# Performance work log

Measured on AMD Instinct MI355X. Metric: run time of the kernel, lower is better.

Reference implementation:

```python
import jax, jax.numpy as jnp
import numpy as np

NODE_DIM = 128
HIDDEN = 64
N_NODES = 2048


def setup_inputs() -> dict:
    key = jax.random.key(0)
    ks = jax.random.split(key, 7)
    s_enc = 1.0 / np.sqrt(NODE_DIM)
    s1 = 1.0 / np.sqrt(2 * HIDDEN)
    s2 = 1.0 / np.sqrt(HIDDEN)
    return {
        "node_features": jax.random.normal(ks[0], (N_NODES, NODE_DIM), dtype=jnp.float32),
        "W_enc": jax.random.uniform(ks[1], (NODE_DIM, HIDDEN), jnp.float32, -s_enc, s_enc),
        "b_enc": jax.random.uniform(ks[2], (HIDDEN,), jnp.float32, -s_enc, s_enc),
        "W1": jax.random.uniform(ks[3], (2 * HIDDEN, HIDDEN), jnp.float32, -s1, s1),
        "b1": jax.random.uniform(ks[4], (HIDDEN,), jnp.float32, -s1, s1),
        "W2": jax.random.uniform(ks[5], (HIDDEN, 1), jnp.float32, -s2, s2),
        "b2": jax.random.uniform(ks[6], (1,), jnp.float32, -s2, s2),
    }


def reference(node_features, W_enc, b_enc, W1, b1, W2, b2):
    # node encoder: (n, node_dim) -> (n, hidden)
    h = node_features @ W_enc + b_enc
    # split first edge-MLP weight into the halves acting on h_i and h_j of the concat
    Wa, Wb = W1[:HIDDEN], W1[HIDDEN:]
    a = h @ Wa  # (n, hidden) contribution from source node i
    b = h @ Wb  # (n, hidden) contribution from target node j
    # pairwise pre-activation: (n, n, hidden) == Linear(concat(h_i, h_j))
    z = jax.nn.relu(a[:, None, :] + b[None, :, :] + b1)
    logits = jnp.einsum("ijh,ho->ijo", z, W2)[..., 0] + b2[0]  # (n, n)
    T = jax.nn.sigmoid(logits)
    # diagonal is never written in the original loop -> stays 0
    n = T.shape[0]
    return T * (1.0 - jnp.eye(n, dtype=T.dtype))
```

## Files before the change

kernel.cpp:

```cpp
#include <hip/hip_runtime.h>
#include <math.h>

#define NODE_DIM 128
#define HIDDEN   64
#define NN       2048

typedef float v4f __attribute__((ext_vector_type(4)));

__global__ __launch_bounds__(256) void prep_kernel(
    const float* __restrict__ nf, const float* __restrict__ W_enc,
    const float* __restrict__ b_enc, const float* __restrict__ W1,
    const float* __restrict__ b1, float* __restrict__ A, float* __restrict__ BB)
{
    __shared__ float nf_s[4][NODE_DIM];
    __shared__ float h_s[4][HIDDEN];
    const int tid = threadIdx.x;
    const int rg  = tid >> 6;
    const int t   = tid & 63;
    const int r   = blockIdx.x * 4 + rg;

    ((float2*)nf_s[rg])[t] = ((const float2*)(nf + (size_t)r * NODE_DIM))[t];
    __syncthreads();

    float acc = b_enc[t];
    #pragma unroll 8
    for (int k = 0; k < NODE_DIM; ++k)
        acc = fmaf(nf_s[rg][k], W_enc[k * HIDDEN + t], acc);
    h_s[rg][t] = acc;
    __syncthreads();

    float aacc = 0.0f;
    float bacc = b1[t];
    #pragma unroll 8
    for (int k = 0; k < HIDDEN; ++k) {
        const float hv = h_s[rg][k];
        aacc = fmaf(hv, W1[k * HIDDEN + t], aacc);
        bacc = fmaf(hv, W1[(HIDDEN + k) * HIDDEN + t], bacc);
    }
    A[(size_t)r * HIDDEN + t]  = aacc;
    BB[(size_t)r * HIDDEN + t] = bacc;
}

__global__ __launch_bounds__(256) void pair_kernel(
    const float* __restrict__ A, const float* __restrict__ BB,
    const float* __restrict__ W2, const float* __restrict__ b2,
    float* __restrict__ out)
{
    __shared__ float aL[64][68];
    __shared__ float bT[64][68];
    __shared__ float w2s[HIDDEN];

    const int tid = threadIdx.x;
    const int i0  = blockIdx.y * 64;
    const int j0  = blockIdx.x * 64;

    const float4* ga = (const float4*)(A  + (size_t)i0 * HIDDEN);
    const float4* gb = (const float4*)(BB + (size_t)j0 * HIDDEN);
    #pragma unroll
    for (int k = 0; k < 4; ++k) {
        const int idx = tid + k * 256;
        const int e   = idx * 4;
        const int row = e >> 6;
        const int col = e & 63;
        const float4 va = ga[idx];
        const float4 vb = gb[idx];
        *(float4*)&aL[row][col] = va;
        bT[col + 0][row] = vb.x;
        bT[col + 1][row] = vb.y;
        bT[col + 2][row] = vb.z;
        bT[col + 3][row] = vb.w;
    }
    if (tid < HIDDEN) w2s[tid] = W2[tid];
    __syncthreads();

    const int ty = tid >> 4;
    const int tx = tid & 15;

    float acc[4][4] = {{0.0f}};

    #pragma unroll 4
    for (int h = 0; h < HIDDEN; h += 4) {
        const v4f w = *(const v4f*)&w2s[h];
        v4f av[4], bv[4];
        #pragma unroll
        for (int ii = 0; ii < 4; ++ii)
            av[ii] = *(const v4f*)&aL[ty * 4 + ii][h];
        #pragma unroll
        for (int hh = 0; hh < 4; ++hh)
            bv[hh] = *(const v4f*)&bT[h + hh][tx * 4];
        #pragma unroll
        for (int ii = 0; ii < 4; ++ii) {
            #pragma unroll
            for (int jj = 0; jj < 4; ++jj) {
                float s = acc[ii][jj];
                #pragma unroll
                for (int hh = 0; hh < 4; ++hh)
                    s = fmaf(fmaxf(av[ii][hh] + bv[hh][jj], 0.0f), w[hh], s);
                acc[ii][jj] = s;
            }
        }
    }

    const float bias2 = b2[0];
    #pragma unroll
    for (int ii = 0; ii < 4; ++ii) {
        const int i = i0 + ty * 4 + ii;
        v4f o;
        #pragma unroll
        for (int jj = 0; jj < 4; ++jj) {
            const int j = j0 + tx * 4 + jj;
            const float x  = acc[ii][jj] + bias2;
            const float sg = 1.0f / (1.0f + __expf(-x));
            o[jj] = (i == j) ? 0.0f : sg;
        }
        *(v4f*)&out[(size_t)i * NN + (j0 + tx * 4)] = o;
    }
}

extern "C" void kernel_launch(void* const* d_in, const int* in_sizes, int n_in,
                              void* d_out, int out_size, void* d_ws, size_t ws_size,
                              hipStream_t stream) {
    const float* nf    = (const float*)d_in[0];
    const float* W_enc = (const float*)d_in[1];
    const float* b_enc = (const float*)d_in[2];
    const float* W1    = (const float*)d_in[3];
    const float* b1    = (const float*)d_in[4];
    const float* W2    = (const float*)d_in[5];
    const float* b2    = (const float*)d_in[6];
    float* out = (float*)d_out;

    float* A  = (float*)d_ws;
    float* BB = A + (size_t)NN * HIDDEN;

    prep_kernel<<<NN / 4, 256, 0, stream>>>(nf, W_enc, b_enc, W1, b1, A, BB);
    pair_kernel<<<dim3(32, 32), 256, 0, stream>>>(A, BB, W2, b2, out);
}
```

Before: 101.3 us.

## Use 128x128 pair tiles with 8x8 per-thread outputs and packed float2 math

The pair kernel moves from 64x64 to 128x128 output tiles, and each thread now computes an 8x8 strided block. The hidden-dimension inner loop uses two-wide vector add, max and multiply, which aims at the packed FP32 instructions, and it keeps two partial sums per output. B is now stored row-major instead of transposed, W2 is read directly from global memory, and launch bounds ask for 2 waves per SIMD. The goal is more arithmetic per shared-memory load and higher ALU throughput, at the cost of many more registers and strided scalar output stores that replace the vectorized stores.

```diff
diff --git a/kernel.cpp b/kernel.cpp
--- a/kernel.cpp
+++ b/kernel.cpp
@@ -4,7 +4,9 @@
 #define NODE_DIM 128
 #define HIDDEN   64
 #define NN       2048
+#define LSTR     68
 
+typedef float v2f __attribute__((ext_vector_type(2)));
 typedef float v4f __attribute__((ext_vector_type(4)));
 
 __global__ __launch_bounds__(256) void prep_kernel(
@@ -41,79 +43,84 @@
     BB[(size_t)r * HIDDEN + t] = bacc;
 }
 
-__global__ __launch_bounds__(256) void pair_kernel(
+__global__ __launch_bounds__(256, 2) void pair_kernel(
     const float* __restrict__ A, const float* __restrict__ BB,
     const float* __restrict__ W2, const float* __restrict__ b2,
     float* __restrict__ out)
 {
-    __shared__ float aL[64][68];
-    __shared__ float bT[64][68];
-    __shared__ float w2s[HIDDEN];
+    __shared__ __align__(16) float aL[128 * LSTR];
+    __shared__ __align__(16) float bL[128 * LSTR];
 
     const int tid = threadIdx.x;
-    const int i0  = blockIdx.y * 64;
-    const int j0  = blockIdx.x * 64;
+    const int i0  = blockIdx.y * 128;
+    const int j0  = blockIdx.x * 128;
 
-    const float4* ga = (const float4*)(A  + (size_t)i0 * HIDDEN);
-    const float4* gb = (const float4*)(BB + (size_t)j0 * HIDDEN);
+    const v4f* gA = (const v4f*)(A  + (size_t)i0 * HIDDEN);
+    const v4f* gB = (const v4f*)(BB + (size_t)j0 * HIDDEN);
     #pragma unroll
-    for (int k = 0; k < 4; ++k) {
+    for (int k = 0; k < 8; ++k) {
         const int idx = tid + k * 256;
-        const int e   = idx * 4;
-        const int row = e >> 6;
-        const int col = e & 63;
-        const float4 va = ga[idx];
-        const float4 vb = gb[idx];
-        *(float4*)&aL[row][col] = va;
-        bT[col + 0][row] = vb.x;
-        bT[col + 1][row] = vb.y;
-        bT[col + 2][row] = vb.z;
-        bT[col + 3][row] = vb.w;
+        const int row = idx >> 4;
+        const int c   = idx & 15;
+        *(v4f*)&aL[row * LSTR + c * 4] = gA[idx];
+        *(v4f*)&bL[row * LSTR + c * 4] = gB[idx];
     }
-    if (tid < HIDDEN) w2s[tid] = W2[tid];
     __syncthreads();
 
     const int ty = tid >> 4;
     const int tx = tid & 15;
 
-    float acc[4][4] = {{0.0f}};
+    v2f acc[8][8];
+    #pragma unroll
+    for (int ii = 0; ii < 8; ++ii)
+        #pragma unroll
+        for (int jj = 0; jj < 8; ++jj)
+            acc[ii][jj] = (v2f){0.0f, 0.0f};
 
-    #pragma unroll 4
-    for (int h = 0; h < HIDDEN; h += 4) {
-        const v4f w = *(const v4f*)&w2s[h];
-        v4f av[4], bv[4];
+    const v2f vz = (v2f){0.0f, 0.0f};
+
+    #pragma unroll 2
+    for (int c = 0; c < 16; ++c) {
+        v4f av[8], bv[8];
         #pragma unroll
-        for (int ii = 0; ii < 4; ++ii)
-            av[ii] = *(const v4f*)&aL[ty * 4 + ii][h];
+        for (int ii = 0; ii < 8; ++ii)
+            av[ii] = *(const v4f*)&aL[(ty + 16 * ii) * LSTR + c * 4];
         #pragma unroll
-        for (int hh = 0; hh < 4; ++hh)
-            bv[hh] = *(const v4f*)&bT[h + hh][tx * 4];
+        for (int jj = 0; jj < 8; ++jj)
+            bv[jj] = *(const v4f*)&bL[(tx + 16 * jj) * LSTR + c * 4];
+
+        const v2f w0 = (v2f){W2[c * 4 + 0], W2[c * 4 + 1]};
+        const v2f w1 = (v2f){W2[c * 4 + 2], W2[c * 4 + 3]};
+
         #pragma unroll
-        for (int ii = 0; ii < 4; ++ii) {
+        for (int ii = 0; ii < 8; ++ii) {
+            const v2f a0 = __builtin_shufflevector(av[ii], av[ii], 0, 1);
+            const v2f a1 = __builtin_shufflevector(av[ii], av[ii], 2, 3);
             #pragma unroll
-            for (int jj = 0; jj < 4; ++jj) {
-                float s = acc[ii][jj];
-                #pragma unroll
-                for (int hh = 0; hh < 4; ++hh)
-                    s = fmaf(fmaxf(av[ii][hh] + bv[hh][jj], 0.0f), w[hh], s);
-                acc[ii][jj] = s;
+            for (int jj = 0; jj < 8; ++jj) {
+                const v2f b0 = __builtin_shufflevector(bv[jj], bv[jj], 0, 1);
+                const v2f b1v = __builtin_shufflevector(bv[jj], bv[jj], 2, 3);
+                v2f t0 = a0 + b0;
+                t0 = __builtin_elementwise_max(t0, vz);
+                acc[ii][jj] += t0 * w0;
+                v2f t1 = a1 + b1v;
+                t1 = __builtin_elementwise_max(t1, vz);
+                acc[ii][jj] += t1 * w1;
             }
         }
     }
 
-    const float bias2 = b2[0];
+    const float b2v = b2[0];
     #pragma unroll
-    for (int ii = 0; ii < 4; ++ii) {
-        const int i = i0 + ty * 4 + ii;
-        v4f o;
+    for (int ii = 0; ii < 8; ++ii) {
+        const int i = i0 + ty + 16 * ii;
         #pragma unroll
-        for (int jj = 0; jj < 4; ++jj) {
-            const int j = j0 + tx * 4 + jj;
-            const float x  = acc[ii][jj] + bias2;
-            const float sg = 1.0f / (1.0f + __expf(-x));
-            o[jj] = (i == j) ? 0.0f : sg;
+        for (int jj = 0; jj < 8; ++jj) {
+            const int j = j0 + tx + 16 * jj;
+            const float lg = acc[ii][jj][0] + acc[ii][jj][1] + b2v;
+            const float sg = 1.0f / (1.0f + __expf(-lg));
+            out[(size_t)i * NN + j] = (i == j) ? 0.0f : sg;
         }
-        *(v4f*)&out[(size_t)i * NN + (j0 + tx * 4)] = o;
     }
 }
 
@@ -133,5 +140,6 @@
     float* BB = A + (size_t)NN * HIDDEN;
 
     prep_kernel<<<NN / 4, 256, 0, stream>>>(nf, W_enc, b_enc, W1, b1, A, BB);
-    pair_kernel<<<dim3(32, 32), 256, 0, stream>>>(A, BB, W2, b2, out);
+    pair_kernel<<<dim3(NN / 128, NN / 128), 256, 0, stream>>>(
+        A, BB, W2, b2, out);
 }
```

Result: no change. 100.7 us (-0.5%).
